# Performance work log

Hardware: AMD Instinct MI355X
Metric: run time of the kernel (lower is better)

The kernel has to match this reference:

```python
import jax, jax.numpy as jnp
import numpy as np

TOPK = 12
D = 256
SCALE = D ** -0.5


def setup_inputs() -> dict:
    key = jax.random.key(0)
    ks = jax.random.split(key, 6)
    N, D_in = 12288, 1024
    def w(k, shape, fan_in):
        return jax.random.normal(k, shape, jnp.float32) / np.float32(np.sqrt(fan_in))
    return {
        "x_path": jax.random.normal(ks[0], (N, D_in), jnp.float32),
        "wsi_w": w(ks[1], (D_in, D), D_in),
        "wsi_b": jnp.zeros((D,), jnp.float32),
        "wh_w": w(ks[2], (D, D), D),
        "wh_b": jnp.zeros((D,), jnp.float32),
        "wt_w": w(ks[3], (D, D), D),
        "wt_b": jnp.zeros((D,), jnp.float32),
        "w1_w": w(ks[4], (D, D), D),
        "w1_b": jnp.zeros((D,), jnp.float32),
        "w2_w": w(ks[5], (D, D), D),
        "w2_b": jnp.zeros((D,), jnp.float32),
    }


def reference(x_path, wsi_w, wsi_b, wh_w, wh_b, wt_w, wt_b, w1_w, w1_b, w2_w, w2_b):
    # wsi_net: Linear(1024,256) + ReLU (dropout is identity in eval)
    h = jax.nn.relu(x_path @ wsi_w + wsi_b)          # [N, D]
    e_h = h @ wh_w + wh_b                            # [N, D]
    e_t = h @ wt_w + wt_b                            # [N, D]
    # dense scaled similarity: [N, N]
    attn_logit = (e_h * SCALE) @ e_t.T
    topk_weight, topk_index = jax.lax.top_k(attn_logit, TOPK)  # [N, K]
    topk_prob = jax.nn.softmax(topk_weight, axis=-1)           # [N, K]
    # gather top-k neighbor tail embeddings
    Nb_h = e_t[topk_index]                           # [N, K, D]
    # eh_r = p * Nb_h + (1-p) (x) e_h   (outer product == broadcast mul)
    eh_r = topk_prob[..., None] * Nb_h + (1.0 - topk_prob)[..., None] * e_h[:, None, :]
    gate = jnp.tanh(e_h[:, None, :] + eh_r)          # [N, K, D]
    ka_weight = jnp.einsum('nkd,nkd->nk', Nb_h, gate)  # [N, K]
    ka_prob = jax.nn.softmax(ka_weight, axis=-1)       # [N, K]
    e_Nh = jnp.einsum('nk,nkd->nd', ka_prob, Nb_h)     # [N, D]
    sum_embedding = jax.nn.relu((e_h + e_Nh) @ w1_w + w1_b)
    bi_embedding = jax.nn.relu((e_h * e_Nh) @ w2_w + w2_b)
    return sum_embedding + bi_embedding              # [N, D]
```

## Files before the change

kernel.cpp:

```cpp
#include <hip/hip_runtime.h>
#include <hip/hip_bf16.h>
#include <cmath>

#define TK 12
#define NROW 12288
#define NEG_BIG (-3.0e38f)
#define MFMA16(a,b,c) __builtin_amdgcn_mfma_f32_16x16x32_f16(a,b,c,0,0,0)

#define NCH 8
#define CTILES 96
#define NPH 48

typedef _Float16 f16x8 __attribute__((ext_vector_type(8)));
typedef _Float16 f16x4 __attribute__((ext_vector_type(4)));
typedef float    f32x4 __attribute__((ext_vector_type(4)));

typedef __attribute__((address_space(1))) const void gvoid_t;
typedef __attribute__((address_space(3))) void lvoid_t;
__device__ __forceinline__ void gload_lds16(const void* g, void* l) {
    __builtin_amdgcn_global_load_lds((gvoid_t*)g, (lvoid_t*)l, 16, 0, 0);
}

__global__ __launch_bounds__(256) void wpack(
    const float* __restrict__ W, _Float16* __restrict__ hi,
    _Float16* __restrict__ lo, int N, int nkt)
{
    const int tid = blockIdx.x * 256 + threadIdx.x;
    const int l = tid & 63;
    const int s = (tid >> 6) % nkt;
    const int cg = tid / (nkt * 64);
    const int krow = s * 32 + 8 * (l >> 4);
    const int col = cg * 16 + (l & 15);
    f16x8 H, L;
    #pragma unroll
    for (int j = 0; j < 8; ++j) {
        float w = W[(size_t)(krow + j) * N + col];
        _Float16 h = (_Float16)w;
        H[j] = h;
        L[j] = (_Float16)(w - (float)h);
    }
    *(f16x8*)(hi + (size_t)tid * 8) = H;
    *(f16x8*)(lo + (size_t)tid * 8) = L;
}

__global__ __launch_bounds__(256) void wpack4(
    const float* __restrict__ W0, const float* __restrict__ W1,
    const float* __restrict__ W2, const float* __restrict__ W3,
    _Float16* __restrict__ base)
{
    const int m = blockIdx.y;
    const float* W = (m == 0) ? W0 : (m == 1) ? W1 : (m == 2) ? W2 : W3;
    _Float16* hi = base + (size_t)m * 131072;
    _Float16* lo = hi + 65536;
    const int tid = blockIdx.x * 256 + threadIdx.x;
    const int l = tid & 63;
    const int s = (tid >> 6) & 7;
    const int cg = tid >> 9;
    const int krow = s * 32 + 8 * (l >> 4);
    const int col = cg * 16 + (l & 15);
    f16x8 H, L;
    #pragma unroll
    for (int j = 0; j < 8; ++j) {
        float w = W[(size_t)(krow + j) * 256 + col];
        _Float16 h = (_Float16)w;
        H[j] = h;
        L[j] = (_Float16)(w - (float)h);
    }
    *(f16x8*)(hi + (size_t)tid * 8) = H;
    *(f16x8*)(lo + (size_t)tid * 8) = L;
}

template<bool RELU>
__global__ __launch_bounds__(256) void gemm_mfma(
    const float* __restrict__ A1,
    const _Float16* __restrict__ Wh, const _Float16* __restrict__ Wl,
    const float* __restrict__ bias, float* __restrict__ C, int K)
{
    __shared__ _Float16 aH[2048], aL[2048];
    __shared__ _Float16 wH[2048], wL[2048];
    const int tid = threadIdx.x, lane = tid & 63, wave = tid >> 6;
    const int rb = blockIdx.y * 64;
    const int cbg = blockIdx.x * 4;
    const int nkt = K >> 5;

    const int arow = rb + wave * 16 + (lane & 15);
    const int acol0 = 8 * (lane >> 4);
    const float* a1p = A1 + (size_t)arow * K + acol0;
    const size_t wbase = ((size_t)(cbg + wave) * nkt) * 512 + lane * 8;

    f32x4 acc[4];
    #pragma unroll
    for (int rg = 0; rg < 4; ++rg) acc[rg] = (f32x4){0.f,0.f,0.f,0.f};

    float4 pa0 = *(const float4*)(a1p);
    float4 pa1 = *(const float4*)(a1p + 4);
    f16x8 pwh = *(const f16x8*)(Wh + wbase);
    f16x8 pwl = *(const f16x8*)(Wl + wbase);

    for (int kt = 0; kt < nkt; ++kt) {
        __syncthreads();
        {
            float v[8] = {pa0.x, pa0.y, pa0.z, pa0.w, pa1.x, pa1.y, pa1.z, pa1.w};
            f16x8 H, L;
            #pragma unroll
            for (int j = 0; j < 8; ++j) {
                _Float16 h = (_Float16)v[j];
                H[j] = h;
                L[j] = (_Float16)(v[j] - (float)h);
            }
            *(f16x8*)&aH[tid*8] = H;
            *(f16x8*)&aL[tid*8] = L;
            *(f16x8*)&wH[tid*8] = pwh;
            *(f16x8*)&wL[tid*8] = pwl;
        }
        __syncthreads();
        if (kt + 1 < nkt) {
            pa0 = *(const float4*)(a1p + (kt+1)*32);
            pa1 = *(const float4*)(a1p + (kt+1)*32 + 4);
            pwh = *(const f16x8*)(Wh + wbase + (size_t)(kt+1)*512);
            pwl = *(const f16x8*)(Wl + wbase + (size_t)(kt+1)*512);
        }
        f16x8 wh = *(const f16x8*)&wH[(wave*64 + lane)*8];
        f16x8 wl = *(const f16x8*)&wL[(wave*64 + lane)*8];
        #pragma unroll
        for (int rg = 0; rg < 4; ++rg) {
            f16x8 ah = *(const f16x8*)&aH[(rg*64 + lane)*8];
            f16x8 al = *(const f16x8*)&aL[(rg*64 + lane)*8];
            acc[rg] = MFMA16(wh, ah, acc[rg]);
            acc[rg] = MFMA16(wl, ah, acc[rg]);
            acc[rg] = MFMA16(wh, al, acc[rg]);
        }
    }
    const int col = (cbg + wave)*16 + 4*(lane >> 4);
    float4 b4 = *(const float4*)(bias + col);
    #pragma unroll
    for (int rg = 0; rg < 4; ++rg) {
        const int row = rb + rg*16 + (lane & 15);
        float4 o;
        o.x = acc[rg][0] + b4.x; o.y = acc[rg][1] + b4.y;
        o.z = acc[rg][2] + b4.z; o.w = acc[rg][3] + b4.w;
        if (RELU) {
            o.x = fmaxf(o.x, 0.f); o.y = fmaxf(o.y, 0.f);
            o.z = fmaxf(o.z, 0.f); o.w = fmaxf(o.w, 0.f);
        }
        *(float4*)(C + (size_t)row*256 + col) = o;
    }
}

template<int DMODE>
__global__ __launch_bounds__(256) void gemm_dual(
    const float* __restrict__ A1, const float* __restrict__ A2,
    const _Float16* __restrict__ W1h, const _Float16* __restrict__ W1l,
    const _Float16* __restrict__ W2h, const _Float16* __restrict__ W2l,
    const float* __restrict__ bias1, const float* __restrict__ bias2,
    float* __restrict__ C1, float* __restrict__ C2,
    _Float16* __restrict__ P1, _Float16* __restrict__ P2)
{
    __shared__ _Float16 aH[2][2048], aL[2][2048];
    __shared__ _Float16 wH[2][2048], wL[2][2048];
    const int tid = threadIdx.x, lane = tid & 63, wave = tid >> 6;
    const int rb = blockIdx.y * 64;
    const int cbg = blockIdx.x * 4;

    const int arow = rb + wave * 16 + (lane & 15);
    const int acol0 = 8 * (lane >> 4);
    const float* a1p = A1 + (size_t)arow * 256 + acol0;
    const float* a2p = (DMODE == 1) ? (A2 + (size_t)arow * 256 + acol0) : nullptr;
    const size_t wbase = ((size_t)(cbg + wave) * 8) * 512 + lane * 8;

    f32x4 acc1[4], acc2[4];
    #pragma unroll
    for (int rg = 0; rg < 4; ++rg) {
        acc1[rg] = (f32x4){0.f,0.f,0.f,0.f};
        acc2[rg] = (f32x4){0.f,0.f,0.f,0.f};
    }

    float4 pa0 = *(const float4*)(a1p);
    float4 pa1 = *(const float4*)(a1p + 4);
    float4 pb0, pb1;
    if (DMODE == 1) { pb0 = *(const float4*)(a2p); pb1 = *(const float4*)(a2p + 4); }
    f16x8 pw1h = *(const f16x8*)(W1h + wbase);
    f16x8 pw1l = *(const f16x8*)(W1l + wbase);
    f16x8 pw2h = *(const f16x8*)(W2h + wbase);
    f16x8 pw2l = *(const f16x8*)(W2l + wbase);

    for (int kt = 0; kt < 8; ++kt) {
        __syncthreads();
        {
            float v[8] = {pa0.x, pa0.y, pa0.z, pa0.w, pa1.x, pa1.y, pa1.z, pa1.w};
            if (DMODE == 0) {
                f16x8 H, L;
                #pragma unroll
                for (int j = 0; j < 8; ++j) {
                    _Float16 h = (_Float16)v[j];
                    H[j] = h;
                    L[j] = (_Float16)(v[j] - (float)h);
                }
                *(f16x8*)&aH[0][tid*8] = H;
                *(f16x8*)&aL[0][tid*8] = L;
            } else {
                float b[8] = {pb0.x, pb0.y, pb0.z, pb0.w, pb1.x, pb1.y, pb1.z, pb1.w};
                f16x8 Hs, Ls, Hm, Lm;
                #pragma unroll
                for (int j = 0; j < 8; ++j) {
                    float s = v[j] + b[j];
                    float m = v[j] * b[j];
                    _Float16 hs = (_Float16)s;
                    _Float16 hm = (_Float16)m;
                    Hs[j] = hs; Ls[j] = (_Float16)(s - (float)hs);
                    Hm[j] = hm; Lm[j] = (_Float16)(m - (float)hm);
                }
                *(f16x8*)&aH[0][tid*8] = Hs;
                *(f16x8*)&aL[0][tid*8] = Ls;
                *(f16x8*)&aH[1][tid*8] = Hm;
                *(f16x8*)&aL[1][tid*8] = Lm;
            }
            *(f16x8*)&wH[0][tid*8] = pw1h;
            *(f16x8*)&wL[0][tid*8] = pw1l;
            *(f16x8*)&wH[1][tid*8] = pw2h;
            *(f16x8*)&wL[1][tid*8] = pw2l;
        }
        __syncthreads();
        if (kt + 1 < 8) {
            pa0 = *(const float4*)(a1p + (kt+1)*32);
            pa1 = *(const float4*)(a1p + (kt+1)*32 + 4);
            if (DMODE == 1) {
                pb0 = *(const float4*)(a2p + (kt+1)*32);
                pb1 = *(const float4*)(a2p + (kt+1)*32 + 4);
            }
            pw1h = *(const f16x8*)(W1h + wbase + (size_t)(kt+1)*512);
            pw1l = *(const f16x8*)(W1l + wbase + (size_t)(kt+1)*512);
            pw2h = *(const f16x8*)(W2h + wbase + (size_t)(kt+1)*512);
            pw2l = *(const f16x8*)(W2l + wbase + (size_t)(kt+1)*512);
        }
        f16x8 w1h = *(const f16x8*)&wH[0][(wave*64 + lane)*8];
        f16x8 w1l = *(const f16x8*)&wL[0][(wave*64 + lane)*8];
        f16x8 w2h = *(const f16x8*)&wH[1][(wave*64 + lane)*8];
        f16x8 w2l = *(const f16x8*)&wL[1][(wave*64 + lane)*8];
        #pragma unroll
        for (int rg = 0; rg < 4; ++rg) {
            f16x8 ah0 = *(const f16x8*)&aH[0][(rg*64 + lane)*8];
            f16x8 al0 = *(const f16x8*)&aL[0][(rg*64 + lane)*8];
            acc1[rg] = MFMA16(w1h, ah0, acc1[rg]);
            acc1[rg] = MFMA16(w1l, ah0, acc1[rg]);
            acc1[rg] = MFMA16(w1h, al0, acc1[rg]);
            f16x8 ah1 = (DMODE == 1) ? *(const f16x8*)&aH[1][(rg*64 + lane)*8] : ah0;
            f16x8 al1 = (DMODE == 1) ? *(const f16x8*)&aL[1][(rg*64 + lane)*8] : al0;
            acc2[rg] = MFMA16(w2h, ah1, acc2[rg]);
            acc2[rg] = MFMA16(w2l, ah1, acc2[rg]);
            acc2[rg] = MFMA16(w2h, al1, acc2[rg]);
        }
    }
    const int col = (cbg + wave)*16 + 4*(lane >> 4);
    float4 b14 = *(const float4*)(bias1 + col);
    float4 b24 = *(const float4*)(bias2 + col);
    #pragma unroll
    for (int rg = 0; rg < 4; ++rg) {
        const int row = rb + rg*16 + (lane & 15);
        if (DMODE == 0) {
            float4 o1, o2;
            o1.x = acc1[rg][0] + b14.x; o1.y = acc1[rg][1] + b14.y;
            o1.z = acc1[rg][2] + b14.z; o1.w = acc1[rg][3] + b14.w;
            o2.x = acc2[rg][0] + b24.x; o2.y = acc2[rg][1] + b24.y;
            o2.z = acc2[rg][2] + b24.z; o2.w = acc2[rg][3] + b24.w;
            *(float4*)(C1 + (size_t)row*256 + col) = o1;
            *(float4*)(C2 + (size_t)row*256 + col) = o2;
            const size_t poff = ((size_t)(row >> 4)*8 + (col >> 5))*512
                              + (((col & 31) >> 3)*16 + (row & 15))*8 + (col & 7);
            f16x4 p1, p2;
            p1[0] = (_Float16)(o1.x * 0.0625f); p1[1] = (_Float16)(o1.y * 0.0625f);
            p1[2] = (_Float16)(o1.z * 0.0625f); p1[3] = (_Float16)(o1.w * 0.0625f);
            p2[0] = (_Float16)o2.x; p2[1] = (_Float16)o2.y;
            p2[2] = (_Float16)o2.z; p2[3] = (_Float16)o2.w;
            *(f16x4*)(P1 + poff) = p1;
            *(f16x4*)(P2 + poff) = p2;
        } else {
            float4 o;
            o.x = fmaxf(acc1[rg][0] + b14.x, 0.f) + fmaxf(acc2[rg][0] + b24.x, 0.f);
            o.y = fmaxf(acc1[rg][1] + b14.y, 0.f) + fmaxf(acc2[rg][1] + b24.y, 0.f);
            o.z = fmaxf(acc1[rg][2] + b14.z, 0.f) + fmaxf(acc2[rg][2] + b24.z, 0.f);
            o.w = fmaxf(acc1[rg][3] + b14.w, 0.f) + fmaxf(acc2[rg][3] + b24.w, 0.f);
            *(float4*)(C1 + (size_t)row*256 + col) = o;
        }
    }
}

__global__ __launch_bounds__(256, 2) void s1_gmax(
    const _Float16* __restrict__ ehh, const _Float16* __restrict__ eth,
    float* __restrict__ tau12)
{
    __shared__ _Float16 abuf[3][8192];
    const int tid = threadIdx.x, lane = tid & 63, wave = tid >> 6;
    const int chunk = blockIdx.x & (NCH-1);
    const int rblk = blockIdx.x >> 3;
    const int rg0 = rblk * 8 + wave * 2;

    f16x8 bh[2][8];
    #pragma unroll
    for (int rs = 0; rs < 2; ++rs) {
        const _Float16* p = ehh + (size_t)(rg0 + rs)*4096 + lane*8;
        #pragma unroll
        for (int s = 0; s < 8; ++s) bh[rs][s] = *(const f16x8*)(p + s*512);
    }
    #pragma unroll
    for (int rs = 0; rs < 2; ++rs)
        #pragma unroll
        for (int s = 0; s < 8; ++s)
            asm volatile("" : "+v"(bh[rs][s]));

    float tv0[TK], tv1[TK];
    #pragma unroll
    for (int j = 0; j < TK; ++j) { tv0[j] = NEG_BIG; tv1[j] = NEG_BIG; }

    const _Float16* gsrc = eth + (size_t)chunk * CTILES * 4096;
    #pragma unroll
    for (int ph = 0; ph < 2; ++ph) {
        #pragma unroll
        for (int i = 0; i < 4; ++i) {
            const int u = wave*4 + i;
            gload_lds16(gsrc + (size_t)(ph*2 + (u>>3))*4096 + (u&7)*512 + lane*8,
                        &abuf[ph][u*512]);
        }
    }
    asm volatile("s_waitcnt vmcnt(4) lgkmcnt(0)" ::: "memory");
    __builtin_amdgcn_s_barrier();
    asm volatile("" ::: "memory");

    int cur = 0;
    for (int p = 0; p < NPH; ++p) {
        int nx = cur + 2; if (nx >= 3) nx -= 3;
        if (p + 2 < NPH) {
            #pragma unroll
            for (int i = 0; i < 4; ++i) {
                const int u = wave*4 + i;
                gload_lds16(gsrc + (size_t)((p+2)*2 + (u>>3))*4096 + (u&7)*512 + lane*8,
                            &abuf[nx][u*512]);
            }
        }
        float gm0 = NEG_BIG, gm1 = NEG_BIG;
        #pragma unroll
        for (int tt = 0; tt < 2; ++tt) {
            f32x4 aE[2], aO[2];
            #pragma unroll
            for (int rs = 0; rs < 2; ++rs) {
                aE[rs] = (f32x4){0.f,0.f,0.f,0.f};
                aO[rs] = (f32x4){0.f,0.f,0.f,0.f};
            }
            #pragma unroll
            for (int s = 0; s < 8; ++s) {
                f16x8 ah = *(const f16x8*)&abuf[cur][tt*4096 + s*512 + lane*8];
                if (s & 1) {
                    aO[0] = MFMA16(ah, bh[0][s], aO[0]);
                    aO[1] = MFMA16(ah, bh[1][s], aO[1]);
                } else {
                    aE[0] = MFMA16(ah, bh[0][s], aE[0]);
                    aE[1] = MFMA16(ah, bh[1][s], aE[1]);
                }
            }
            f32x4 a0 = aE[0] + aO[0];
            f32x4 a1 = aE[1] + aO[1];
            gm0 = fmaxf(gm0, fmaxf(fmaxf(a0[0],a0[1]), fmaxf(a0[2],a0[3])));
            gm1 = fmaxf(gm1, fmaxf(fmaxf(a1[0],a1[1]), fmaxf(a1[2],a1[3])));
        }
        gm0 = fmaxf(gm0, __shfl_xor(gm0, 16)); gm0 = fmaxf(gm0, __shfl_xor(gm0, 32));
        gm1 = fmaxf(gm1, __shfl_xor(gm1, 16)); gm1 = fmaxf(gm1, __shfl_xor(gm1, 32));
        #pragma unroll
        for (int j = TK-1; j >= 1; --j)
            tv0[j] = __builtin_amdgcn_fmed3f(gm0, tv0[j], tv0[j-1]);
        tv0[0] = fmaxf(gm0, tv0[0]);
        #pragma unroll
        for (int j = TK-1; j >= 1; --j)
            tv1[j] = __builtin_amdgcn_fmed3f(gm1, tv1[j], tv1[j-1]);
        tv1[0] = fmaxf(gm1, tv1[0]);

        if (p + 2 < NPH) { asm volatile("s_waitcnt vmcnt(4)" ::: "memory"); }
        else             { asm volatile("s_waitcnt vmcnt(0)" ::: "memory"); }
        __builtin_amdgcn_s_barrier();
        asm volatile("" ::: "memory");
        cur = cur + 1; if (cur >= 3) cur = 0;
    }

    if (lane < 16) {
        const int row0 = rg0 * 16 + lane;
        float* op0 = tau12 + ((size_t)chunk*NROW + row0)*TK;
        float* op1 = tau12 + ((size_t)chunk*NROW + row0 + 16)*TK;
        #pragma unroll
        for (int j = 0; j < TK; ++j) { op0[j] = tv0[j]; op1[j] = tv1[j]; }
    }
}

__global__ __launch_bounds__(256) void b1_tau(
    const float* __restrict__ tau12, float* __restrict__ tau)
{
    const int row = blockIdx.x * 256 + threadIdx.x;
    float tv[TK];
    #pragma unroll
    for (int j = 0; j < TK; ++j) tv[j] = NEG_BIG;
    #pragma unroll 1
    for (int c = 0; c < NCH; ++c) {
        const float* p = tau12 + ((size_t)c*NROW + row)*TK;
        float4 q0 = *(const float4*)p;
        float4 q1 = *(const float4*)(p + 4);
        float4 q2 = *(const float4*)(p + 8);
        float vv[TK] = {q0.x,q0.y,q0.z,q0.w, q1.x,q1.y,q1.z,q1.w, q2.x,q2.y,q2.z,q2.w};
        #pragma unroll
        for (int i = 0; i < TK; ++i) {
            float v = vv[i];
            #pragma unroll
            for (int j = TK-1; j >= 1; --j)
                tv[j] = __builtin_amdgcn_fmed3f(v, tv[j], tv[j-1]);
            tv[0] = fmaxf(v, tv[0]);
        }
    }
    tau[row] = tv[TK-1] - 0.02f;
}

#define S2CAP 1024
__global__ __launch_bounds__(256, 2) void s2_collect(
    const _Float16* __restrict__ ehh, const _Float16* __restrict__ eth,
    const float* __restrict__ tau, unsigned int* __restrict__ cnt,
    int* __restrict__ cand)
{
    __shared__ _Float16 abuf[3][8192];
    __shared__ int cmeta[S2CAP];
    __shared__ unsigned int lcnt;
    const int tid = threadIdx.x, lane = tid & 63, wave = tid >> 6;
    const int chunk = blockIdx.x & (NCH-1);
    const int rblk = blockIdx.x >> 3;
    const int rg0 = rblk * 8 + wave * 2;
    if (tid == 0) lcnt = 0;

    f16x8 bh[2][8];
    #pragma unroll
    for (int rs = 0; rs < 2; ++rs) {
        const _Float16* p = ehh + (size_t)(rg0 + rs)*4096 + lane*8;
        #pragma unroll
        for (int s = 0; s < 8; ++s) bh[rs][s] = *(const f16x8*)(p + s*512);
    }
    #pragma unroll
    for (int rs = 0; rs < 2; ++rs)
        #pragma unroll
        for (int s = 0; s < 8; ++s)
            asm volatile("" : "+v"(bh[rs][s]));

    const float tau0 = tau[rblk*128 + wave*32 + (lane & 15)];
    const float tau1 = tau[rblk*128 + wave*32 + 16 + (lane & 15)];

    const _Float16* gsrc = eth + (size_t)chunk * CTILES * 4096;
    #pragma unroll
    for (int ph = 0; ph < 2; ++ph) {
        #pragma unroll
        for (int i = 0; i < 4; ++i) {
            const int u = wave*4 + i;
            gload_lds16(gsrc + (size_t)(ph*2 + (u>>3))*4096 + (u&7)*512 + lane*8,
                        &abuf[ph][u*512]);
        }
    }
    asm volatile("s_waitcnt vmcnt(4) lgkmcnt(0)" ::: "memory");
    __builtin_amdgcn_s_barrier();
    asm volatile("" ::: "memory");

    int cur = 0;
    for (int p = 0; p < NPH; ++p) {
        int nx = cur + 2; if (nx >= 3) nx -= 3;
        if (p + 2 < NPH) {
            #pragma unroll
            for (int i = 0; i < 4; ++i) {
                const int u = wave*4 + i;
                gload_lds16(gsrc + (size_t)((p+2)*2 + (u>>3))*4096 + (u&7)*512 + lane*8,
                            &abuf[nx][u*512]);
            }
        }
        #pragma unroll
        for (int tt = 0; tt < 2; ++tt) {
            f32x4 aE[2], aO[2];
            #pragma unroll
            for (int rs = 0; rs < 2; ++rs) {
                aE[rs] = (f32x4){0.f,0.f,0.f,0.f};
                aO[rs] = (f32x4){0.f,0.f,0.f,0.f};
            }
            #pragma unroll
            for (int s = 0; s < 8; ++s) {
                f16x8 ah = *(const f16x8*)&abuf[cur][tt*4096 + s*512 + lane*8];
                if (s & 1) {
                    aO[0] = MFMA16(ah, bh[0][s], aO[0]);
                    aO[1] = MFMA16(ah, bh[1][s], aO[1]);
                } else {
                    aE[0] = MFMA16(ah, bh[0][s], aE[0]);
                    aE[1] = MFMA16(ah, bh[1][s], aE[1]);
                }
            }
            const int cb = (chunk*CTILES + p*2 + tt)*16 + 4*(lane >> 4);
            f32x4 a0 = aE[0] + aO[0];
            f32x4 a1 = aE[1] + aO[1];
            float m0 = fmaxf(fmaxf(a0[0],a0[1]), fmaxf(a0[2],a0[3]));
            float m1 = fmaxf(fmaxf(a1[0],a1[1]), fmaxf(a1[2],a1[3]));
            if (__any(m0 >= tau0 || m1 >= tau1)) {
                const int lrow = wave*32 + (lane & 15);
                #pragma unroll
                for (int e = 0; e < 4; ++e) {
                    if (a0[e] >= tau0) {
                        unsigned q = atomicAdd(&lcnt, 1u);
                        if (q < S2CAP) cmeta[q] = (cb + e) | (lrow << 16);
                    }
                    if (a1[e] >= tau1) {
                        unsigned q = atomicAdd(&lcnt, 1u);
                        if (q < S2CAP) cmeta[q] = (cb + e) | ((lrow + 16) << 16);
                    }
                }
            }
        }
        if (p + 2 < NPH) { asm volatile("s_waitcnt vmcnt(4)" ::: "memory"); }
        else             { asm volatile("s_waitcnt vmcnt(0)" ::: "memory"); }
        __builtin_amdgcn_s_barrier();
        asm volatile("" ::: "memory");
        cur = cur + 1; if (cur >= 3) cur = 0;
    }
    asm volatile("s_waitcnt lgkmcnt(0)" ::: "memory");
    __builtin_amdgcn_s_barrier();
    asm volatile("" ::: "memory");
    const int row0 = rblk * 128;
    const unsigned n = (lcnt < (unsigned)S2CAP) ? lcnt : (unsigned)S2CAP;
    for (unsigned i = tid; i < n; i += 256) {
        const int m = cmeta[i];
        const int row = row0 + (m >> 16);
        unsigned q = atomicAdd(&cnt[row], 1u);
        if (q < 64) cand[(size_t)row*64 + q] = m & 0xffff;
    }
}

__global__ __launch_bounds__(256) void s3_tail(
    const float* __restrict__ e_h, const float* __restrict__ e_t,
    const unsigned int* __restrict__ cnt, const int* __restrict__ cand,
    float* __restrict__ e_Nh)
{
    const int lane = threadIdx.x & 63;
    const int wave = threadIdx.x >> 6;
    const int row  = blockIdx.x * 4 + wave;

    const unsigned cn = min(cnt[row], 64u);
    const bool act = lane < (int)cn;
    int colc = act ? cand[(size_t)row*64 + lane] : 0x7fffffff;

    const float* ehr = e_h + (size_t)row * 256;
    const float* etr = e_t + (size_t)(act ? colc : 0) * 256;
    float s = 0.f;
    for (int k = 0; k < 64; ++k) {
        float4 a = *(const float4*)(ehr + k*4);
        float4 b = *(const float4*)(etr + k*4);
        s += a.x*b.x + a.y*b.y + a.z*b.z + a.w*b.w;
    }
    s *= 0.0625f;
    if (!act) s = NEG_BIG;

    float tvv[TK]; int ti[TK];
    float v = s; int c = colc;
    #pragma unroll
    for (int o = 0; o < TK; ++o) {
        float bv = v; int bc = c;
        #pragma unroll
        for (int off = 32; off; off >>= 1) {
            float ov = __shfl_xor(bv, off);
            int   oc = __shfl_xor(bc, off);
            bool take = (ov > bv) || (ov == bv && oc < bc);
            bv = take ? ov : bv;
            bc = take ? oc : bc;
        }
        tvv[o] = bv; ti[o] = bc;
        if (c == bc) v = NEG_BIG;
    }

    float p[TK]; float Z = 0.f;
    #pragma unroll
    for (int j = 0; j < TK; ++j) { p[j] = expf(tvv[j] - tvv[0]); Z += p[j]; }
    const float invZ = 1.f / Z;
    #pragma unroll
    for (int j = 0; j < TK; ++j) p[j] *= invZ;

    float4 eh = *(const float4*)(ehr + lane * 4);

    float4 nb[TK]; float kw[TK];
    #pragma unroll
    for (int k = 0; k < TK; ++k) {
        float4 n = *(const float4*)(e_t + (size_t)ti[k] * 256 + lane * 4);
        nb[k] = n;
        const float pk = p[k], qk = 1.f - p[k];
        float4 gt;
        gt.x = tanhf(eh.x + (pk * n.x + qk * eh.x));
        gt.y = tanhf(eh.y + (pk * n.y + qk * eh.y));
        gt.z = tanhf(eh.z + (pk * n.z + qk * eh.z));
        gt.w = tanhf(eh.w + (pk * n.w + qk * eh.w));
        float d = n.x*gt.x + n.y*gt.y + n.z*gt.z + n.w*gt.w;
        #pragma unroll
        for (int off = 32; off; off >>= 1) d += __shfl_xor(d, off);
        kw[k] = d;
    }

    float km = kw[0];
    #pragma unroll
    for (int k = 1; k < TK; ++k) km = fmaxf(km, kw[k]);
    float kz = 0.f; float kp[TK];
    #pragma unroll
    for (int k = 0; k < TK; ++k) { kp[k] = expf(kw[k] - km); kz += kp[k]; }
    const float invKZ = 1.f / kz;

    float4 acc = make_float4(0.f, 0.f, 0.f, 0.f);
    #pragma unroll
    for (int k = 0; k < TK; ++k) {
        acc.x += kp[k] * nb[k].x;
        acc.y += kp[k] * nb[k].y;
        acc.z += kp[k] * nb[k].z;
        acc.w += kp[k] * nb[k].w;
    }
    acc.x *= invKZ; acc.y *= invKZ; acc.z *= invKZ; acc.w *= invKZ;
    *(float4*)(e_Nh + (size_t)row * 256 + lane * 4) = acc;
}

extern "C" void kernel_launch(void* const* d_in, const int* in_sizes, int n_in,
                              void* d_out, int out_size, void* d_ws, size_t ws_size,
                              hipStream_t stream)
{
    (void)in_sizes; (void)n_in; (void)out_size; (void)ws_size;
    const float* x     = (const float*)d_in[0];
    const float* wsi_w = (const float*)d_in[1];
    const float* wsi_b = (const float*)d_in[2];
    const float* wh_w  = (const float*)d_in[3];
    const float* wh_b  = (const float*)d_in[4];
    const float* wt_w  = (const float*)d_in[5];
    const float* wt_b  = (const float*)d_in[6];
    const float* w1_w  = (const float*)d_in[7];
    const float* w1_b  = (const float*)d_in[8];
    const float* w2_w  = (const float*)d_in[9];
    const float* w2_b  = (const float*)d_in[10];
    float* out = (float*)d_out;
    float* ws  = (float*)d_ws;

    const int M = NROW;
    const size_t ND = (size_t)M * 256;

    float* h    = ws;
    float* e_h  = ws + ND;
    float* e_t  = ws + 2*ND;
    _Float16* ehh = (_Float16*)(ws + 3*ND);
    _Float16* eth = (_Float16*)(ws + 3*ND + ND/2);
    size_t o = 4*ND;
    float* tau12 = ws + o;                        o += (size_t)NCH*NROW*TK;
    float* tau = ws + o;                          o += NROW;
    unsigned int* cnt = (unsigned int*)(ws + o);  o += NROW;
    int* cand = (int*)(ws + o);                   o += (size_t)NROW*64;
    _Float16* hp = (_Float16*)(ws + o);
    _Float16* wsiH = hp;
    _Float16* wsiL = hp + 262144;
    _Float16* w4base = hp + 524288;
    _Float16* whH  = w4base;
    _Float16* whL  = w4base + 65536;
    _Float16* wtH  = w4base + 2*65536;
    _Float16* wtL  = w4base + 3*65536;
    _Float16* w1H  = w4base + 4*65536;
    _Float16* w1L  = w4base + 5*65536;
    _Float16* w2H  = w4base + 6*65536;
    _Float16* w2L  = w4base + 7*65536;
    float* e_Nh = h;

    wpack<<<128, 256, 0, stream>>>(wsi_w, wsiH, wsiL, 256, 32);
    wpack4<<<dim3(32, 4), 256, 0, stream>>>(wh_w, wt_w, w1_w, w2_w, w4base);

    gemm_mfma<true><<<dim3(4, M/64), 256, 0, stream>>>(
        x, wsiH, wsiL, wsi_b, h, 1024);
    gemm_dual<0><<<dim3(4, M/64), 256, 0, stream>>>(
        h, nullptr, whH, whL, wtH, wtL, wh_b, wt_b, e_h, e_t, ehh, eth);
    s1_gmax<<<NCH*96, 256, 0, stream>>>(ehh, eth, tau12);
    b1_tau<<<M/256, 256, 0, stream>>>(tau12, tau);
    hipMemsetAsync(cnt, 0, (size_t)M*sizeof(unsigned int), stream);
    s2_collect<<<NCH*96, 256, 0, stream>>>(ehh, eth, tau, cnt, cand);
    s3_tail<<<M/4, 256, 0, stream>>>(e_h, e_t, cnt, cand, e_Nh);
    gemm_dual<1><<<dim3(4, M/64), 256, 0, stream>>>(
        e_h, e_Nh, w1H, w1L, w2H, w2L, w1_b, w2_b, out, nullptr, nullptr, nullptr);
}
```

Before: 360.4 us.

## Replace second similarity pass with per-group top-2 summaries and candidate emission

The first similarity pass now records, for each row and each 32-column group, the top two maxima as packed fp16 plus the column index of the maximum. A new lightweight kernel derives the threshold from these group maxima and emits candidate columns directly, which removes the second full MFMA pass over the N×N similarity (s2_collect), the memset and the atomics. In exchange s1 writes more global data per phase, the candidate cap grows to 256, and s3 rescoring handles up to 256 candidates per row. Groups whose second max also passes the threshold emit all 32 columns, which may inflate candidate counts, and fp16 rounding of the summaries affects threshold precision.

```diff
diff --git a/kernel.cpp b/kernel.cpp
--- a/kernel.cpp
+++ b/kernel.cpp
@@ -10,6 +10,7 @@
 #define NCH 8
 #define CTILES 96
 #define NPH 48
+#define CAP 256
 
 typedef _Float16 f16x8 __attribute__((ext_vector_type(8)));
 typedef _Float16 f16x4 __attribute__((ext_vector_type(4)));
@@ -287,7 +288,7 @@
 
 __global__ __launch_bounds__(256, 2) void s1_gmax(
     const _Float16* __restrict__ ehh, const _Float16* __restrict__ eth,
-    float* __restrict__ tau12)
+    unsigned* __restrict__ g32, unsigned char* __restrict__ gcol)
 {
     __shared__ _Float16 abuf[3][8192];
     const int tid = threadIdx.x, lane = tid & 63, wave = tid >> 6;
@@ -307,10 +308,6 @@
         #pragma unroll
         for (int s = 0; s < 8; ++s)
             asm volatile("" : "+v"(bh[rs][s]));
-
-    float tv0[TK], tv1[TK];
-    #pragma unroll
-    for (int j = 0; j < TK; ++j) { tv0[j] = NEG_BIG; tv1[j] = NEG_BIG; }
 
     const _Float16* gsrc = eth + (size_t)chunk * CTILES * 4096;
     #pragma unroll
@@ -337,7 +334,8 @@
                             &abuf[nx][u*512]);
             }
         }
-        float gm0 = NEG_BIG, gm1 = NEG_BIG;
+        float m1a = NEG_BIG, m2a = NEG_BIG; int mca = 0;
+        float m1b = NEG_BIG, m2b = NEG_BIG; int mcb = 0;
         #pragma unroll
         for (int tt = 0; tt < 2; ++tt) {
             f32x4 aE[2], aO[2];
@@ -359,174 +357,94 @@
             }
             f32x4 a0 = aE[0] + aO[0];
             f32x4 a1 = aE[1] + aO[1];
-            gm0 = fmaxf(gm0, fmaxf(fmaxf(a0[0],a0[1]), fmaxf(a0[2],a0[3])));
-            gm1 = fmaxf(gm1, fmaxf(fmaxf(a1[0],a1[1]), fmaxf(a1[2],a1[3])));
-        }
-        gm0 = fmaxf(gm0, __shfl_xor(gm0, 16)); gm0 = fmaxf(gm0, __shfl_xor(gm0, 32));
-        gm1 = fmaxf(gm1, __shfl_xor(gm1, 16)); gm1 = fmaxf(gm1, __shfl_xor(gm1, 32));
-        #pragma unroll
-        for (int j = TK-1; j >= 1; --j)
-            tv0[j] = __builtin_amdgcn_fmed3f(gm0, tv0[j], tv0[j-1]);
-        tv0[0] = fmaxf(gm0, tv0[0]);
-        #pragma unroll
-        for (int j = TK-1; j >= 1; --j)
-            tv1[j] = __builtin_amdgcn_fmed3f(gm1, tv1[j], tv1[j-1]);
-        tv1[0] = fmaxf(gm1, tv1[0]);
-
-        if (p + 2 < NPH) { asm volatile("s_waitcnt vmcnt(4)" ::: "memory"); }
+            const int cb = tt*16 + 4*(lane >> 4);
+            #pragma unroll
+            for (int e = 0; e < 4; ++e) {
+                bool g0 = a0[e] > m1a;
+                m2a = fmaxf(m2a, g0 ? m1a : a0[e]);
+                mca = g0 ? (cb + e) : mca;
+                m1a = fmaxf(m1a, a0[e]);
+                bool g1 = a1[e] > m1b;
+                m2b = fmaxf(m2b, g1 ? m1b : a1[e]);
+                mcb = g1 ? (cb + e) : mcb;
+                m1b = fmaxf(m1b, a1[e]);
+            }
+        }
+        #pragma unroll
+        for (int k = 16; k <= 32; k <<= 1) {
+            float o1 = __shfl_xor(m1a, k); int oc = __shfl_xor(mca, k);
+            float o2 = __shfl_xor(m2a, k);
+            bool gt = o1 > m1a;
+            m2a = fmaxf(fmaxf(m2a, o2), gt ? m1a : o1);
+            mca = gt ? oc : mca;
+            m1a = fmaxf(m1a, o1);
+            float p1 = __shfl_xor(m1b, k); int pc = __shfl_xor(mcb, k);
+            float p2 = __shfl_xor(m2b, k);
+            bool ht = p1 > m1b;
+            m2b = fmaxf(fmaxf(m2b, p2), ht ? m1b : p1);
+            mcb = ht ? pc : mcb;
+            m1b = fmaxf(m1b, p1);
+        }
+        if (lane < 32) {
+            const int rsw = lane >> 4;
+            float M1 = rsw ? m1b : m1a;
+            float M2 = rsw ? m2b : m2a;
+            int   MC = rsw ? mcb : mca;
+            unsigned short h1 = __builtin_bit_cast(unsigned short, (_Float16)M1);
+            unsigned short h2 = __builtin_bit_cast(unsigned short, (_Float16)M2);
+            const int row = (rg0 + rsw)*16 + (lane & 15);
+            const size_t gi = (size_t)(chunk*NPH + p)*NROW + row;
+            g32[gi]  = ((unsigned)h1 << 16) | h2;
+            gcol[gi] = (unsigned char)MC;
+        }
+        if (p + 2 < NPH) { asm volatile("s_waitcnt vmcnt(6)" ::: "memory"); }
         else             { asm volatile("s_waitcnt vmcnt(0)" ::: "memory"); }
         __builtin_amdgcn_s_barrier();
         asm volatile("" ::: "memory");
         cur = cur + 1; if (cur >= 3) cur = 0;
     }
-
-    if (lane < 16) {
-        const int row0 = rg0 * 16 + lane;
-        float* op0 = tau12 + ((size_t)chunk*NROW + row0)*TK;
-        float* op1 = tau12 + ((size_t)chunk*NROW + row0 + 16)*TK;
-        #pragma unroll
-        for (int j = 0; j < TK; ++j) { op0[j] = tv0[j]; op1[j] = tv1[j]; }
-    }
-}
-
-__global__ __launch_bounds__(256) void b1_tau(
-    const float* __restrict__ tau12, float* __restrict__ tau)
+}
+
+__global__ __launch_bounds__(256) void b2_emit(
+    const unsigned* __restrict__ g32, const unsigned char* __restrict__ gcol,
+    unsigned* __restrict__ cnt, int* __restrict__ cand)
 {
     const int row = blockIdx.x * 256 + threadIdx.x;
     float tv[TK];
     #pragma unroll
     for (int j = 0; j < TK; ++j) tv[j] = NEG_BIG;
-    #pragma unroll 1
-    for (int c = 0; c < NCH; ++c) {
-        const float* p = tau12 + ((size_t)c*NROW + row)*TK;
-        float4 q0 = *(const float4*)p;
-        float4 q1 = *(const float4*)(p + 4);
-        float4 q2 = *(const float4*)(p + 8);
-        float vv[TK] = {q0.x,q0.y,q0.z,q0.w, q1.x,q1.y,q1.z,q1.w, q2.x,q2.y,q2.z,q2.w};
-        #pragma unroll
-        for (int i = 0; i < TK; ++i) {
-            float v = vv[i];
-            #pragma unroll
-            for (int j = TK-1; j >= 1; --j)
-                tv[j] = __builtin_amdgcn_fmed3f(v, tv[j], tv[j-1]);
-            tv[0] = fmaxf(v, tv[0]);
-        }
-    }
-    tau[row] = tv[TK-1] - 0.02f;
-}
-
-#define S2CAP 1024
-__global__ __launch_bounds__(256, 2) void s2_collect(
-    const _Float16* __restrict__ ehh, const _Float16* __restrict__ eth,
-    const float* __restrict__ tau, unsigned int* __restrict__ cnt,
-    int* __restrict__ cand)
-{
-    __shared__ _Float16 abuf[3][8192];
-    __shared__ int cmeta[S2CAP];
-    __shared__ unsigned int lcnt;
-    const int tid = threadIdx.x, lane = tid & 63, wave = tid >> 6;
-    const int chunk = blockIdx.x & (NCH-1);
-    const int rblk = blockIdx.x >> 3;
-    const int rg0 = rblk * 8 + wave * 2;
-    if (tid == 0) lcnt = 0;
-
-    f16x8 bh[2][8];
-    #pragma unroll
-    for (int rs = 0; rs < 2; ++rs) {
-        const _Float16* p = ehh + (size_t)(rg0 + rs)*4096 + lane*8;
-        #pragma unroll
-        for (int s = 0; s < 8; ++s) bh[rs][s] = *(const f16x8*)(p + s*512);
-    }
-    #pragma unroll
-    for (int rs = 0; rs < 2; ++rs)
-        #pragma unroll
-        for (int s = 0; s < 8; ++s)
-            asm volatile("" : "+v"(bh[rs][s]));
-
-    const float tau0 = tau[rblk*128 + wave*32 + (lane & 15)];
-    const float tau1 = tau[rblk*128 + wave*32 + 16 + (lane & 15)];
-
-    const _Float16* gsrc = eth + (size_t)chunk * CTILES * 4096;
-    #pragma unroll
-    for (int ph = 0; ph < 2; ++ph) {
-        #pragma unroll
-        for (int i = 0; i < 4; ++i) {
-            const int u = wave*4 + i;
-            gload_lds16(gsrc + (size_t)(ph*2 + (u>>3))*4096 + (u&7)*512 + lane*8,
-                        &abuf[ph][u*512]);
-        }
-    }
-    asm volatile("s_waitcnt vmcnt(4) lgkmcnt(0)" ::: "memory");
-    __builtin_amdgcn_s_barrier();
-    asm volatile("" ::: "memory");
-
-    int cur = 0;
-    for (int p = 0; p < NPH; ++p) {
-        int nx = cur + 2; if (nx >= 3) nx -= 3;
-        if (p + 2 < NPH) {
-            #pragma unroll
-            for (int i = 0; i < 4; ++i) {
-                const int u = wave*4 + i;
-                gload_lds16(gsrc + (size_t)((p+2)*2 + (u>>3))*4096 + (u&7)*512 + lane*8,
-                            &abuf[nx][u*512]);
-            }
-        }
-        #pragma unroll
-        for (int tt = 0; tt < 2; ++tt) {
-            f32x4 aE[2], aO[2];
-            #pragma unroll
-            for (int rs = 0; rs < 2; ++rs) {
-                aE[rs] = (f32x4){0.f,0.f,0.f,0.f};
-                aO[rs] = (f32x4){0.f,0.f,0.f,0.f};
-            }
-            #pragma unroll
-            for (int s = 0; s < 8; ++s) {
-                f16x8 ah = *(const f16x8*)&abuf[cur][tt*4096 + s*512 + lane*8];
-                if (s & 1) {
-                    aO[0] = MFMA16(ah, bh[0][s], aO[0]);
-                    aO[1] = MFMA16(ah, bh[1][s], aO[1]);
+    #pragma unroll 4
+    for (int g = 0; g < NCH*NPH; ++g) {
+        unsigned u = g32[(size_t)g*NROW + row];
+        float m1 = (float)__builtin_bit_cast(_Float16, (unsigned short)(u >> 16));
+        #pragma unroll
+        for (int j = TK-1; j >= 1; --j)
+            tv[j] = __builtin_amdgcn_fmed3f(m1, tv[j], tv[j-1]);
+        tv[0] = fmaxf(m1, tv[0]);
+    }
+    const float tau = tv[TK-1] - 0.02f;
+    int n = 0;
+    int* crow = cand + (size_t)row * CAP;
+    for (int ch = 0; ch < NCH; ++ch) {
+        #pragma unroll 4
+        for (int p = 0; p < NPH; ++p) {
+            const int g = ch*NPH + p;
+            unsigned u = g32[(size_t)g*NROW + row];
+            float m1 = (float)__builtin_bit_cast(_Float16, (unsigned short)(u >> 16));
+            if (m1 >= tau) {
+                const int cbase = ch*1536 + p*32;
+                float m2 = (float)__builtin_bit_cast(_Float16, (unsigned short)(u & 0xffffu));
+                if (m2 >= tau) {
+                    #pragma unroll 1
+                    for (int c = 0; c < 32; ++c)
+                        if (n < CAP) crow[n++] = cbase + c;
                 } else {
-                    aE[0] = MFMA16(ah, bh[0][s], aE[0]);
-                    aE[1] = MFMA16(ah, bh[1][s], aE[1]);
+                    if (n < CAP) crow[n++] = cbase + (int)gcol[(size_t)g*NROW + row];
                 }
             }
-            const int cb = (chunk*CTILES + p*2 + tt)*16 + 4*(lane >> 4);
-            f32x4 a0 = aE[0] + aO[0];
-            f32x4 a1 = aE[1] + aO[1];
-            float m0 = fmaxf(fmaxf(a0[0],a0[1]), fmaxf(a0[2],a0[3]));
-            float m1 = fmaxf(fmaxf(a1[0],a1[1]), fmaxf(a1[2],a1[3]));
-            if (__any(m0 >= tau0 || m1 >= tau1)) {
-                const int lrow = wave*32 + (lane & 15);
-                #pragma unroll
-                for (int e = 0; e < 4; ++e) {
-                    if (a0[e] >= tau0) {
-                        unsigned q = atomicAdd(&lcnt, 1u);
-                        if (q < S2CAP) cmeta[q] = (cb + e) | (lrow << 16);
-                    }
-                    if (a1[e] >= tau1) {
-                        unsigned q = atomicAdd(&lcnt, 1u);
-                        if (q < S2CAP) cmeta[q] = (cb + e) | ((lrow + 16) << 16);
-                    }
-                }
-            }
-        }
-        if (p + 2 < NPH) { asm volatile("s_waitcnt vmcnt(4)" ::: "memory"); }
-        else             { asm volatile("s_waitcnt vmcnt(0)" ::: "memory"); }
-        __builtin_amdgcn_s_barrier();
-        asm volatile("" ::: "memory");
-        cur = cur + 1; if (cur >= 3) cur = 0;
-    }
-    asm volatile("s_waitcnt lgkmcnt(0)" ::: "memory");
-    __builtin_amdgcn_s_barrier();
-    asm volatile("" ::: "memory");
-    const int row0 = rblk * 128;
-    const unsigned n = (lcnt < (unsigned)S2CAP) ? lcnt : (unsigned)S2CAP;
-    for (unsigned i = tid; i < n; i += 256) {
-        const int m = cmeta[i];
-        const int row = row0 + (m >> 16);
-        unsigned q = atomicAdd(&cnt[row], 1u);
-        if (q < 64) cand[(size_t)row*64 + q] = m & 0xffff;
-    }
+        }
+    }
+    cnt[row] = (unsigned)n;
 }
 
 __global__ __launch_bounds__(256) void s3_tail(
@@ -538,26 +456,38 @@
     const int wave = threadIdx.x >> 6;
     const int row  = blockIdx.x * 4 + wave;
 
-    const unsigned cn = min(cnt[row], 64u);
-    const bool act = lane < (int)cn;
-    int colc = act ? cand[(size_t)row*64 + lane] : 0x7fffffff;
-
+    const unsigned cn = min(cnt[row], (unsigned)CAP);
     const float* ehr = e_h + (size_t)row * 256;
-    const float* etr = e_t + (size_t)(act ? colc : 0) * 256;
-    float s = 0.f;
-    for (int k = 0; k < 64; ++k) {
-        float4 a = *(const float4*)(ehr + k*4);
-        float4 b = *(const float4*)(etr + k*4);
-        s += a.x*b.x + a.y*b.y + a.z*b.z + a.w*b.w;
-    }
-    s *= 0.0625f;
-    if (!act) s = NEG_BIG;
+
+    float v[4]; int c[4];
+    #pragma unroll
+    for (int i = 0; i < 4; ++i) {
+        const int idx = lane + 64*i;
+        const bool act = idx < (int)cn;
+        c[i] = act ? cand[(size_t)row*CAP + idx] : (0x7ffffff0 + i);
+        v[i] = NEG_BIG;
+        if ((int)cn > 64*i) {
+            const float* etr = e_t + (size_t)(act ? c[i] : 0) * 256;
+            float s = 0.f;
+            for (int k = 0; k < 64; ++k) {
+                float4 a = *(const float4*)(ehr + k*4);
+                float4 b = *(const float4*)(etr + k*4);
+                s += a.x*b.x + a.y*b.y + a.z*b.z + a.w*b.w;
+            }
+            if (act) v[i] = s * 0.0625f;
+        }
+    }
 
     float tvv[TK]; int ti[TK];
-    float v = s; int c = colc;
     #pragma unroll
     for (int o = 0; o < TK; ++o) {
-        float bv = v; int bc = c;
+        float bv = v[0]; int bc = c[0];
+        #pragma unroll
+        for (int i = 1; i < 4; ++i) {
+            bool take = (v[i] > bv) || (v[i] == bv && c[i] < bc);
+            bv = take ? v[i] : bv;
+            bc = take ? c[i] : bc;
+        }
         #pragma unroll
         for (int off = 32; off; off >>= 1) {
             float ov = __shfl_xor(bv, off);
@@ -567,7 +497,9 @@
             bc = take ? oc : bc;
         }
         tvv[o] = bv; ti[o] = bc;
-        if (c == bc) v = NEG_BIG;
+        #pragma unroll
+        for (int i = 0; i < 4; ++i)
+            if (c[i] == bc) v[i] = NEG_BIG;
     }
 
     float p[TK]; float Z = 0.f;
@@ -644,10 +576,10 @@
     _Float16* ehh = (_Float16*)(ws + 3*ND);
     _Float16* eth = (_Float16*)(ws + 3*ND + ND/2);
     size_t o = 4*ND;
-    float* tau12 = ws + o;                        o += (size_t)NCH*NROW*TK;
-    float* tau = ws + o;                          o += NROW;
+    unsigned* g32 = (unsigned*)(ws + o);          o += (size_t)NCH*NPH*NROW;
+    unsigned char* gcol = (unsigned char*)(ws + o); o += (size_t)NCH*NPH*NROW/4;
     unsigned int* cnt = (unsigned int*)(ws + o);  o += NROW;
-    int* cand = (int*)(ws + o);                   o += (size_t)NROW*64;
+    int* cand = (int*)(ws + o);                   o += (size_t)NROW*CAP;
     _Float16* hp = (_Float16*)(ws + o);
     _Float16* wsiH = hp;
     _Float16* wsiL = hp + 262144;
@@ -669,10 +601,8 @@
         x, wsiH, wsiL, wsi_b, h, 1024);
     gemm_dual<0><<<dim3(4, M/64), 256, 0, stream>>>(
         h, nullptr, whH, whL, wtH, wtL, wh_b, wt_b, e_h, e_t, ehh, eth);
-    s1_gmax<<<NCH*96, 256, 0, stream>>>(ehh, eth, tau12);
-    b1_tau<<<M/256, 256, 0, stream>>>(tau12, tau);
-    hipMemsetAsync(cnt, 0, (size_t)M*sizeof(unsigned int), stream);
-    s2_collect<<<NCH*96, 256, 0, stream>>>(ehh, eth, tau, cnt, cand);
+    s1_gmax<<<NCH*96, 256, 0, stream>>>(ehh, eth, g32, gcol);
+    b2_emit<<<M/256, 256, 0, stream>>>(g32, gcol, cnt, cand);
     s3_tail<<<M/4, 256, 0, stream>>>(e_h, e_t, cnt, cand, e_Nh);
     gemm_dual<1><<<dim3(4, M/64), 256, 0, stream>>>(
         e_h, e_Nh, w1H, w1L, w2H, w2L, w1_b, w2_b, out, nullptr, nullptr, nullptr);
```

Result: slower. 493.0 us (+36.8%).
